# Kernel tuning notes

Hardware: AMD Instinct MI355X
Metric: run time of the kernel (lower is better)

Reference implementation:

```python
import jax, jax.numpy as jnp
import numpy as np

N = 100000
E = 3200000
IN_DIM = 512
HID = [64, 32, 16]
OUT_DIM = 40
BN_EPS = 1e-5


def setup_inputs() -> dict:
    key = jax.random.key(0)
    ks = jax.random.split(key, 10)
    x = jax.random.normal(ks[0], (N, IN_DIM), dtype=jnp.float32)
    edge_row = jnp.sort(jax.random.randint(ks[1], (E,), 0, N, dtype=jnp.int32))
    edge_col = jax.random.randint(ks[2], (E,), 0, N, dtype=jnp.int32)
    edge_val = jax.random.uniform(ks[3], (E,), dtype=jnp.float32)

    def xavier(k, fan_in, fan_out):
        limit = np.sqrt(6.0 / (fan_in + fan_out)).astype(np.float32)
        return jax.random.uniform(k, (fan_in, fan_out), dtype=jnp.float32, minval=-limit, maxval=limit)

    W1 = xavier(ks[4], IN_DIM, HID[0])
    W2 = xavier(ks[5], HID[0], HID[1])
    W3 = xavier(ks[6], HID[1], HID[2])
    W4 = xavier(ks[7], HID[2], OUT_DIM)
    return {
        "x": x, "edge_row": edge_row, "edge_col": edge_col, "edge_val": edge_val,
        "W1": W1, "W2": W2, "W3": W3, "W4": W4,
        "g1": jnp.ones((HID[0],), jnp.float32), "b1": jnp.zeros((HID[0],), jnp.float32),
        "g2": jnp.ones((HID[1],), jnp.float32), "b2": jnp.zeros((HID[1],), jnp.float32),
        "g3": jnp.ones((HID[2],), jnp.float32), "b3": jnp.zeros((HID[2],), jnp.float32),
    }


def _gcn_layer(h, W, edge_row, edge_col, edge_val, n_nodes):
    # support = h @ W  (dense GEMM), then SpMM: out[i] = sum_{e: row[e]=i} val[e] * support[col[e]]
    support = h @ W
    msgs = edge_val[:, None] * support[edge_col]  # gather + scale
    return jax.ops.segment_sum(msgs, edge_row, num_segments=n_nodes)


def _bn_elu(h, gamma, beta):
    # BatchNorm1d in training mode: batch statistics over the node dim, biased variance
    mean = jnp.mean(h, axis=0)
    var = jnp.var(h, axis=0)
    h = (h - mean) * jax.lax.rsqrt(var + BN_EPS) * gamma + beta
    return jax.nn.elu(h)


def reference(x, edge_row, edge_col, edge_val, W1, W2, W3, W4, g1, b1, g2, b2, g3, b3):
    n = x.shape[0]
    h = _gcn_layer(x, W1, edge_row, edge_col, edge_val, n)
    h = _bn_elu(h, g1, b1)  # dropout is identity in eval mode
    h = _gcn_layer(h, W2, edge_row, edge_col, edge_val, n)
    h = _bn_elu(h, g2, b2)
    h = _gcn_layer(h, W3, edge_row, edge_col, edge_val, n)
    h = _bn_elu(h, g3, b3)
    h = _gcn_layer(h, W4, edge_row, edge_col, edge_val, n)
    return jax.nn.log_softmax(h, axis=1)
```

## Files before the change

### kernel.cpp

```cpp
#include <hip/hip_runtime.h>
#include <hip/hip_bf16.h>
#include <math.h>

typedef __attribute__((ext_vector_type(8))) short short8;
typedef __attribute__((ext_vector_type(4))) float floatx4;

__global__ void rowptr_k(const int* __restrict__ erow, int* __restrict__ rp, int n, int e) {
    int i = blockIdx.x * blockDim.x + threadIdx.x;
    if (i > n) return;
    int lo = 0, hi = e;
    while (lo < hi) {
        int mid = (lo + hi) >> 1;
        if (erow[mid] < i) lo = mid + 1; else hi = mid;
    }
    rp[i] = lo;
}

__global__ void zero_k(float* __restrict__ p) {
    int i = threadIdx.x;
    if (i < 224) p[i] = 0.f;
}

__device__ __forceinline__ float elu_f(float t) {
    return t > 0.f ? t : expm1f(t);
}

__device__ __forceinline__ unsigned short f2bf(float f) {
    unsigned int u = __float_as_uint(f);
    u = (u + 0x7FFFu + ((u >> 16) & 1u)) >> 16;
    return (unsigned short)u;
}

__device__ __forceinline__ unsigned int f2bf2(float lo, float hi) {
    unsigned int a = __float_as_uint(lo);
    unsigned int b = __float_as_uint(hi);
    a = (a + 0x7FFFu + ((a >> 16) & 1u)) >> 16;
    b = (b + 0x7FFFu + ((b >> 16) & 1u)) & 0xFFFF0000u;
    return a | b;
}

__device__ __forceinline__ float bflo(unsigned int d) { return __uint_as_float(d << 16); }
__device__ __forceinline__ float bfhi(unsigned int d) { return __uint_as_float(d & 0xFFFF0000u); }

__global__ __launch_bounds__(256) void w1bf_k(const float* __restrict__ W,
                                              unsigned short* __restrict__ Wb) {
    int idx = blockIdx.x * 256 + threadIdx.x;
    int n = idx >> 9, k = idx & 511;
    Wb[idx] = f2bf(W[(long)k * 64 + n]);
}

__global__ __launch_bounds__(256) void wsmall_k(const float* __restrict__ W2,
                                                const float* __restrict__ W3,
                                                const float* __restrict__ W4,
                                                unsigned short* __restrict__ Wb2,
                                                unsigned short* __restrict__ Wb3,
                                                unsigned short* __restrict__ Wb4) {
    int idx = blockIdx.x * 256 + threadIdx.x;
    if (idx < 2048) {
        int n = idx >> 6, k = idx & 63;
        Wb2[idx] = f2bf(W2[(long)k * 32 + n]);
    }
    if (idx < 512) {
        int n = idx >> 5, k = idx & 31;
        Wb3[idx] = f2bf(W3[(long)k * 16 + n]);
    }
    if (idx < 1536) {
        int n = idx >> 5, k = idx & 31;
        Wb4[idx] = (n < 40 && k < 16) ? f2bf(W4[(long)k * 40 + n]) : (unsigned short)0;
    }
}

__global__ __launch_bounds__(256) void gemm1_mfma_k(const float* __restrict__ X,
                                                    const unsigned short* __restrict__ Wb,
                                                    unsigned short* __restrict__ out, int nrows) {
    const int lane = threadIdx.x & 63;
    const int wid  = threadIdx.x >> 6;
    const int lrow = lane & 15;
    const int quad = lane >> 4;
    const int m0   = (blockIdx.x * 4 + wid) * 16;
    if (m0 >= nrows) return;

    int arow = m0 + lrow;
    if (arow >= nrows) arow = nrows - 1;
    const float* __restrict__ xrow = X + (long)arow * 512 + quad * 8;
    const unsigned short* __restrict__ brow = Wb + lrow * 512 + quad * 8;

    floatx4 acc[4];
#pragma unroll
    for (int ni = 0; ni < 4; ++ni) acc[ni] = (floatx4){0.f, 0.f, 0.f, 0.f};

    float4 ca0 = *(const float4*)(xrow + 0);
    float4 ca1 = *(const float4*)(xrow + 4);
    short8 cb[4];
#pragma unroll
    for (int ni = 0; ni < 4; ++ni) cb[ni] = *(const short8*)(brow + ni * 8192);

#pragma unroll
    for (int kc = 0; kc < 16; ++kc) {
        float4 na0, na1;
        short8 nb[4];
        if (kc < 15) {
            const float* xp = xrow + (kc + 1) * 32;
            na0 = *(const float4*)(xp + 0);
            na1 = *(const float4*)(xp + 4);
#pragma unroll
            for (int ni = 0; ni < 4; ++ni)
                nb[ni] = *(const short8*)(brow + ni * 8192 + (kc + 1) * 32);
        }
        union { short8 s; unsigned int u[4]; } af;
        af.u[0] = f2bf2(ca0.x, ca0.y);
        af.u[1] = f2bf2(ca0.z, ca0.w);
        af.u[2] = f2bf2(ca1.x, ca1.y);
        af.u[3] = f2bf2(ca1.z, ca1.w);
#pragma unroll
        for (int ni = 0; ni < 4; ++ni)
            acc[ni] = __builtin_amdgcn_mfma_f32_16x16x32_bf16(af.s, cb[ni], acc[ni], 0, 0, 0);
        if (kc < 15) {
            ca0 = na0; ca1 = na1;
#pragma unroll
            for (int ni = 0; ni < 4; ++ni) cb[ni] = nb[ni];
        }
    }

#pragma unroll
    for (int r = 0; r < 4; ++r) {
        int gr = m0 + quad * 4 + r;
        if (gr < nrows) {
#pragma unroll
            for (int ni = 0; ni < 4; ++ni)
                out[(long)gr * 64 + ni * 16 + lrow] = f2bf(acc[ni][r]);
        }
    }
}

template<int K, int KP, int NF, int NSTR>
__global__ __launch_bounds__(256) void gemmS_k(const unsigned short* __restrict__ H,
                                               const unsigned short* __restrict__ Wb,
                                               const float* __restrict__ stats,
                                               const float* __restrict__ gamma,
                                               const float* __restrict__ beta,
                                               unsigned short* __restrict__ out,
                                               int nrows) {
    __shared__ __align__(16) float scs[K];
    __shared__ __align__(16) float shs[K];
    const int tid = threadIdx.x;
    if (tid < K) {
        float s1 = stats[tid], s2 = stats[K + tid];
        float mean = s1 / (float)nrows;
        float var  = s2 / (float)nrows - mean * mean;
        float rstd = rsqrtf(var + 1e-5f);
        float scl  = gamma[tid] * rstd;
        scs[tid] = scl;
        shs[tid] = beta[tid] - mean * scl;
    }
    __syncthreads();

    const int lane = tid & 63;
    const int wid  = tid >> 6;
    const int lrow = lane & 15;
    const int quad = lane >> 4;
    const int m0   = (blockIdx.x * 4 + wid) * 16;
    if (m0 >= nrows) return;

    int arow = m0 + lrow;
    if (arow >= nrows) arow = nrows - 1;
    const unsigned short* __restrict__ hrow = H + (long)arow * K;

    floatx4 acc[NF];
#pragma unroll
    for (int ni = 0; ni < NF; ++ni) acc[ni] = (floatx4){0.f, 0.f, 0.f, 0.f};

#pragma unroll
    for (int kc = 0; kc < KP; kc += 32) {
        const int k8 = kc + quad * 8;
        union { short8 s; unsigned int u[4]; } af;
        if (k8 < K) {
            uint4 d = *(const uint4*)(hrow + k8);
            float4 sc0 = *(const float4*)&scs[k8];
            float4 sc1 = *(const float4*)&scs[k8 + 4];
            float4 sh0 = *(const float4*)&shs[k8];
            float4 sh1 = *(const float4*)&shs[k8 + 4];
            float f0 = elu_f(bflo(d.x) * sc0.x + sh0.x);
            float f1 = elu_f(bfhi(d.x) * sc0.y + sh0.y);
            float f2 = elu_f(bflo(d.y) * sc0.z + sh0.z);
            float f3 = elu_f(bfhi(d.y) * sc0.w + sh0.w);
            float f4 = elu_f(bflo(d.z) * sc1.x + sh1.x);
            float f5 = elu_f(bfhi(d.z) * sc1.y + sh1.y);
            float f6 = elu_f(bflo(d.w) * sc1.z + sh1.z);
            float f7 = elu_f(bfhi(d.w) * sc1.w + sh1.w);
            af.u[0] = f2bf2(f0, f1);
            af.u[1] = f2bf2(f2, f3);
            af.u[2] = f2bf2(f4, f5);
            af.u[3] = f2bf2(f6, f7);
        } else {
            af.u[0] = af.u[1] = af.u[2] = af.u[3] = 0u;
        }
#pragma unroll
        for (int ni = 0; ni < NF; ++ni) {
            short8 bf = *(const short8*)&Wb[(ni * 16 + lrow) * KP + k8];
            acc[ni] = __builtin_amdgcn_mfma_f32_16x16x32_bf16(af.s, bf, acc[ni], 0, 0, 0);
        }
    }

#pragma unroll
    for (int r = 0; r < 4; ++r) {
        int gr = m0 + quad * 4 + r;
        if (gr < nrows) {
#pragma unroll
            for (int ni = 0; ni < NF; ++ni)
                out[(long)gr * NSTR + ni * 16 + lrow] = f2bf(acc[ni][r]);
        }
    }
}

template<int F>
__global__ __launch_bounds__(256) void spmmb_k(const int* __restrict__ rp,
                                               const int* __restrict__ ecol,
                                               const float* __restrict__ ev,
                                               const unsigned short* __restrict__ sup,
                                               unsigned short* __restrict__ out, int n) {
    constexpr int GL = F / 4;
    constexpr int G  = 64 / GL;
    const int lane = threadIdx.x & 63;
    const int node = (blockIdx.x * blockDim.x + threadIdx.x) >> 6;
    if (node >= n) return;
    int s = __builtin_amdgcn_readfirstlane(rp[node]);
    int e = __builtin_amdgcn_readfirstlane(rp[node + 1]);
    const int g = lane / GL, p = lane % GL;
    float a0 = 0.f, a1 = 0.f, a2 = 0.f, a3 = 0.f;
    for (int i = s; i < e; i += 4 * G) {
#pragma unroll
        for (int b = 0; b < 4; ++b) {
            int idx = i + b * G + g;
            int cidx = idx < e ? idx : e - 1;
            int col = ecol[cidx];
            float v = ev[cidx];
            if (idx >= e) v = 0.f;
            uint2 d = *(const uint2*)((const char*)sup + (unsigned long long)col * (F * 2) + p * 8);
            a0 += v * bflo(d.x);
            a1 += v * bfhi(d.x);
            a2 += v * bflo(d.y);
            a3 += v * bfhi(d.y);
        }
    }
#pragma unroll
    for (int o = GL; o < 64; o <<= 1) {
        a0 += __shfl_xor(a0, o, 64);
        a1 += __shfl_xor(a1, o, 64);
        a2 += __shfl_xor(a2, o, 64);
        a3 += __shfl_xor(a3, o, 64);
    }
    if (lane < GL) {
        ushort4 o4;
        o4.x = f2bf(a0); o4.y = f2bf(a1); o4.z = f2bf(a2); o4.w = f2bf(a3);
        *(ushort4*)&out[(long)node * F + p * 4] = o4;
    }
}

__global__ __launch_bounds__(256) void spmm4b_k(const int* __restrict__ rp,
                                                const int* __restrict__ ecol,
                                                const float* __restrict__ ev,
                                                const unsigned short* __restrict__ sup,
                                                float* __restrict__ out, int n) {
    const int lane = threadIdx.x & 63;
    const int node = (blockIdx.x * blockDim.x + threadIdx.x) >> 6;
    if (node >= n) return;
    int s = __builtin_amdgcn_readfirstlane(rp[node]);
    int e = __builtin_amdgcn_readfirstlane(rp[node + 1]);
    const int g = lane >> 4, p = lane & 15;
    float a0 = 0.f, a1 = 0.f, a2 = 0.f, a3 = 0.f;
    for (int i = s; i < e; i += 16) {
#pragma unroll
        for (int b = 0; b < 4; ++b) {
            int idx = i + b * 4 + g;
            int cidx = idx < e ? idx : e - 1;
            int col = ecol[cidx];
            float v = ev[cidx];
            if (idx >= e || p >= 12) v = 0.f;
            uint2 d = *(const uint2*)((const char*)sup + (unsigned long long)col * 96 + p * 8);
            a0 += v * bflo(d.x);
            a1 += v * bfhi(d.x);
            a2 += v * bflo(d.y);
            a3 += v * bfhi(d.y);
        }
    }
#pragma unroll
    for (int o = 16; o < 64; o <<= 1) {
        a0 += __shfl_xor(a0, o, 64);
        a1 += __shfl_xor(a1, o, 64);
        a2 += __shfl_xor(a2, o, 64);
        a3 += __shfl_xor(a3, o, 64);
    }
    const bool valid = p < 10;
    float lm = valid ? fmaxf(fmaxf(a0, a1), fmaxf(a2, a3)) : -INFINITY;
#pragma unroll
    for (int o = 1; o < 16; o <<= 1) lm = fmaxf(lm, __shfl_xor(lm, o, 64));
    float ls = valid ? (expf(a0 - lm) + expf(a1 - lm) + expf(a2 - lm) + expf(a3 - lm)) : 0.f;
#pragma unroll
    for (int o = 1; o < 16; o <<= 1) ls += __shfl_xor(ls, o, 64);
    float lse = lm + logf(ls);
    if (lane < 10) {
        float4 o4 = make_float4(a0 - lse, a1 - lse, a2 - lse, a3 - lse);
        *(float4*)&out[(long)node * 40 + p * 4] = o4;
    }
}

template<int F>
__global__ __launch_bounds__(256) void statsb_k(const unsigned short* __restrict__ h,
                                                float* __restrict__ stats, int n) {
    __shared__ float m1[256], m2[256], m3[256], m4[256];
    const int tid = threadIdx.x;
    const unsigned int* h2 = (const unsigned int*)h;
    const long total = (long)n * F / 2;
    float s1 = 0.f, s2 = 0.f, t1 = 0.f, t2 = 0.f;
    for (long idx = (long)blockIdx.x * 256 + tid; idx < total; idx += (long)gridDim.x * 256) {
        unsigned int d = h2[idx];
        float lo = bflo(d), hi = bfhi(d);
        s1 += lo; s2 += lo * lo;
        t1 += hi; t2 += hi * hi;
    }
    m1[tid] = s1; m2[tid] = s2; m3[tid] = t1; m4[tid] = t2;
    __syncthreads();
    if (tid < F / 2) {
#pragma unroll 4
        for (int j = 1; j < 256 / (F / 2); ++j) {
            s1 += m1[tid + j * (F / 2)];
            s2 += m2[tid + j * (F / 2)];
            t1 += m3[tid + j * (F / 2)];
            t2 += m4[tid + j * (F / 2)];
        }
        atomicAdd(&stats[2 * tid], s1);
        atomicAdd(&stats[2 * tid + 1], t1);
        atomicAdd(&stats[F + 2 * tid], s2);
        atomicAdd(&stats[F + 2 * tid + 1], t2);
    }
}

extern "C" void kernel_launch(void* const* d_in, const int* in_sizes, int n_in,
                              void* d_out, int out_size, void* d_ws, size_t ws_size,
                              hipStream_t stream) {
    const float* x    = (const float*)d_in[0];
    const int*   erow = (const int*)d_in[1];
    const int*   ecol = (const int*)d_in[2];
    const float* ev   = (const float*)d_in[3];
    const float* W1   = (const float*)d_in[4];
    const float* W2   = (const float*)d_in[5];
    const float* W3   = (const float*)d_in[6];
    const float* W4   = (const float*)d_in[7];
    const float* g1   = (const float*)d_in[8];
    const float* b1   = (const float*)d_in[9];
    const float* g2   = (const float*)d_in[10];
    const float* b2   = (const float*)d_in[11];
    const float* g3   = (const float*)d_in[12];
    const float* b3   = (const float*)d_in[13];

    const int N = in_sizes[0] / 512;
    const int E = in_sizes[1];

    char* w = (char*)d_ws;
    int* rp = (int*)w;
    size_t off = (((size_t)(N + 1) * 4) + 255) & ~(size_t)255;
    float* stats = (float*)(w + off);
    unsigned short* Abf = (unsigned short*)(stats + 256);
    unsigned short* Bbf = Abf + (size_t)N * 64;
    unsigned short* Wb1 = Bbf + (size_t)N * 64;
    unsigned short* Wb2 = Wb1 + 64 * 512;
    unsigned short* Wb3 = Wb2 + 32 * 64;
    unsigned short* Wb4 = Wb3 + 16 * 32;
    float* outp = (float*)d_out;

    rowptr_k<<<(N + 1 + 255) / 256, 256, 0, stream>>>(erow, rp, N, E);
    zero_k<<<1, 256, 0, stream>>>(stats);
    w1bf_k<<<128, 256, 0, stream>>>(W1, Wb1);
    wsmall_k<<<8, 256, 0, stream>>>(W2, W3, W4, Wb2, Wb3, Wb4);

    const int mblocks = ((N + 15) / 16 + 3) / 4;
    const int sblocks = (N * 64 + 255) / 256;

    gemm1_mfma_k<<<mblocks, 256, 0, stream>>>(x, Wb1, Abf, N);
    spmmb_k<64><<<sblocks, 256, 0, stream>>>(rp, ecol, ev, Abf, Bbf, N);
    statsb_k<64><<<512, 256, 0, stream>>>(Bbf, stats, N);

    gemmS_k<64, 64, 2, 32><<<mblocks, 256, 0, stream>>>(Bbf, Wb2, stats, g1, b1, Abf, N);
    spmmb_k<32><<<sblocks, 256, 0, stream>>>(rp, ecol, ev, Abf, Bbf, N);
    statsb_k<32><<<512, 256, 0, stream>>>(Bbf, stats + 128, N);

    gemmS_k<32, 32, 1, 16><<<mblocks, 256, 0, stream>>>(Bbf, Wb3, stats + 128, g2, b2, Abf, N);
    spmmb_k<16><<<sblocks, 256, 0, stream>>>(rp, ecol, ev, Abf, Bbf, N);
    statsb_k<16><<<512, 256, 0, stream>>>(Bbf, stats + 192, N);

    gemmS_k<16, 32, 3, 48><<<mblocks, 256, 0, stream>>>(Bbf, Wb4, stats + 192, g3, b3, Abf, N);
    spmm4b_k<<<sblocks, 256, 0, stream>>>(rp, ecol, ev, Abf, outp, N);
}
```

Before: 668.8 us.

## Reorder last layer to aggregate 16-wide features before applying W4

The final layer now runs the sparse aggregation on the 16-wide BN+ELU activations, with normalization fused into the gather, and applies W4 plus log-softmax afterwards in a small dense kernel. This uses (A·h)·W = A·(h·W), so each edge gathers 32 bytes per neighbour instead of 96 and the padded 48-wide support GEMM is no longer needed. In exchange, ELU and the BN affine are recomputed for every gathered edge, and a 16-wide float intermediate is written and read back. Edge processing widens to 16 edges per iteration, with 4 lanes per edge.

Result: slower. 683.6 us (+2.2%).

```diff
diff --git a/kernel.cpp b/kernel.cpp
--- a/kernel.cpp
+++ b/kernel.cpp
@@ -51,10 +51,8 @@
 
 __global__ __launch_bounds__(256) void wsmall_k(const float* __restrict__ W2,
                                                 const float* __restrict__ W3,
-                                                const float* __restrict__ W4,
                                                 unsigned short* __restrict__ Wb2,
-                                                unsigned short* __restrict__ Wb3,
-                                                unsigned short* __restrict__ Wb4) {
+                                                unsigned short* __restrict__ Wb3) {
     int idx = blockIdx.x * 256 + threadIdx.x;
     if (idx < 2048) {
         int n = idx >> 6, k = idx & 63;
@@ -63,10 +61,6 @@
     if (idx < 512) {
         int n = idx >> 5, k = idx & 31;
         Wb3[idx] = f2bf(W3[(long)k * 16 + n]);
-    }
-    if (idx < 1536) {
-        int n = idx >> 5, k = idx & 31;
-        Wb4[idx] = (n < 40 && k < 16) ? f2bf(W4[(long)k * 40 + n]) : (unsigned short)0;
     }
 }
 
@@ -257,40 +251,87 @@
     }
 }
 
-__global__ __launch_bounds__(256) void spmm4b_k(const int* __restrict__ rp,
-                                                const int* __restrict__ ecol,
-                                                const float* __restrict__ ev,
-                                                const unsigned short* __restrict__ sup,
-                                                float* __restrict__ out, int n) {
+__global__ __launch_bounds__(256) void spmmf16_k(const int* __restrict__ rp,
+                                                 const int* __restrict__ ecol,
+                                                 const float* __restrict__ ev,
+                                                 const unsigned short* __restrict__ h,
+                                                 const float* __restrict__ stats,
+                                                 const float* __restrict__ gamma,
+                                                 const float* __restrict__ beta,
+                                                 float* __restrict__ out, int n) {
     const int lane = threadIdx.x & 63;
     const int node = (blockIdx.x * blockDim.x + threadIdx.x) >> 6;
     if (node >= n) return;
+    const int g = lane >> 2, p = lane & 3;
+    float scl[4], sh[4];
+#pragma unroll
+    for (int j = 0; j < 4; ++j) {
+        int c = p * 4 + j;
+        float s1 = stats[c], s2 = stats[16 + c];
+        float mean = s1 / (float)n;
+        float var  = s2 / (float)n - mean * mean;
+        float rstd = rsqrtf(var + 1e-5f);
+        scl[j] = gamma[c] * rstd;
+        sh[j]  = beta[c] - mean * scl[j];
+    }
     int s = __builtin_amdgcn_readfirstlane(rp[node]);
     int e = __builtin_amdgcn_readfirstlane(rp[node + 1]);
-    const int g = lane >> 4, p = lane & 15;
     float a0 = 0.f, a1 = 0.f, a2 = 0.f, a3 = 0.f;
-    for (int i = s; i < e; i += 16) {
+    for (int i = s; i < e; i += 64) {
 #pragma unroll
         for (int b = 0; b < 4; ++b) {
-            int idx = i + b * 4 + g;
+            int idx = i + b * 16 + g;
             int cidx = idx < e ? idx : e - 1;
             int col = ecol[cidx];
             float v = ev[cidx];
-            if (idx >= e || p >= 12) v = 0.f;
-            uint2 d = *(const uint2*)((const char*)sup + (unsigned long long)col * 96 + p * 8);
-            a0 += v * bflo(d.x);
-            a1 += v * bfhi(d.x);
-            a2 += v * bflo(d.y);
-            a3 += v * bfhi(d.y);
-        }
-    }
-#pragma unroll
-    for (int o = 16; o < 64; o <<= 1) {
+            if (idx >= e) v = 0.f;
+            uint2 d = *(const uint2*)((const char*)h + (unsigned long long)col * 32 + p * 8);
+            a0 += v * elu_f(bflo(d.x) * scl[0] + sh[0]);
+            a1 += v * elu_f(bfhi(d.x) * scl[1] + sh[1]);
+            a2 += v * elu_f(bflo(d.y) * scl[2] + sh[2]);
+            a3 += v * elu_f(bfhi(d.y) * scl[3] + sh[3]);
+        }
+    }
+#pragma unroll
+    for (int o = 4; o < 64; o <<= 1) {
         a0 += __shfl_xor(a0, o, 64);
         a1 += __shfl_xor(a1, o, 64);
         a2 += __shfl_xor(a2, o, 64);
         a3 += __shfl_xor(a3, o, 64);
     }
+    if (lane < 4) {
+        float4 o4 = make_float4(a0, a1, a2, a3);
+        *(float4*)&out[(long)node * 16 + p * 4] = o4;
+    }
+}
+
+__global__ __launch_bounds__(256) void gemm4ls_k(const float* __restrict__ T,
+                                                 const float* __restrict__ W4,
+                                                 float* __restrict__ out, int n) {
+    __shared__ __align__(16) float w[16 * 64];
+    const int tid = threadIdx.x;
+    for (int i = tid; i < 1024; i += 256) {
+        int k = i >> 6, c = i & 63;
+        w[i] = (c < 40) ? W4[k * 40 + c] : 0.f;
+    }
+    __syncthreads();
+    const int grp = tid >> 4;
+    const int p   = tid & 15;
+    const int row = blockIdx.x * 16 + grp;
+    if (row >= n) return;
+    const float4* tp = (const float4*)(T + (long)row * 16);
+    float4 t0 = tp[0], t1 = tp[1], t2 = tp[2], t3 = tp[3];
+    float h[16] = {t0.x, t0.y, t0.z, t0.w, t1.x, t1.y, t1.z, t1.w,
+                   t2.x, t2.y, t2.z, t2.w, t3.x, t3.y, t3.z, t3.w};
+    float a0 = 0.f, a1 = 0.f, a2 = 0.f, a3 = 0.f;
+#pragma unroll
+    for (int k = 0; k < 16; ++k) {
+        float4 wv = *(const float4*)&w[k * 64 + p * 4];
+        a0 += h[k] * wv.x;
+        a1 += h[k] * wv.y;
+        a2 += h[k] * wv.z;
+        a3 += h[k] * wv.w;
+    }
     const bool valid = p < 10;
     float lm = valid ? fmaxf(fmaxf(a0, a1), fmaxf(a2, a3)) : -INFINITY;
 #pragma unroll
@@ -299,9 +340,9 @@
 #pragma unroll
     for (int o = 1; o < 16; o <<= 1) ls += __shfl_xor(ls, o, 64);
     float lse = lm + logf(ls);
-    if (lane < 10) {
+    if (valid) {
         float4 o4 = make_float4(a0 - lse, a1 - lse, a2 - lse, a3 - lse);
-        *(float4*)&out[(long)node * 40 + p * 4] = o4;
+        *(float4*)&out[(long)row * 40 + p * 4] = o4;
     }
 }
 
@@ -366,13 +407,13 @@
     unsigned short* Wb1 = Bbf + (size_t)N * 64;
     unsigned short* Wb2 = Wb1 + 64 * 512;
     unsigned short* Wb3 = Wb2 + 32 * 64;
-    unsigned short* Wb4 = Wb3 + 16 * 32;
+    float* Tf = (float*)Abf;
     float* outp = (float*)d_out;
 
     rowptr_k<<<(N + 1 + 255) / 256, 256, 0, stream>>>(erow, rp, N, E);
     zero_k<<<1, 256, 0, stream>>>(stats);
     w1bf_k<<<128, 256, 0, stream>>>(W1, Wb1);
-    wsmall_k<<<8, 256, 0, stream>>>(W2, W3, W4, Wb2, Wb3, Wb4);
+    wsmall_k<<<8, 256, 0, stream>>>(W2, W3, Wb2, Wb3);
 
     const int mblocks = ((N + 15) / 16 + 3) / 4;
     const int sblocks = (N * 64 + 255) / 256;
@@ -389,6 +430,6 @@
     spmmb_k<16><<<sblocks, 256, 0, stream>>>(rp, ecol, ev, Abf, Bbf, N);
     statsb_k<16><<<512, 256, 0, stream>>>(Bbf, stats + 192, N);
 
-    gemmS_k<16, 32, 3, 48><<<mblocks, 256, 0, stream>>>(Bbf, Wb4, stats + 192, g3, b3, Abf, N);
-    spmm4b_k<<<sblocks, 256, 0, stream>>>(rp, ecol, ev, Abf, outp, N);
-}
+    spmmf16_k<<<sblocks, 256, 0, stream>>>(rp, ecol, ev, Bbf, stats + 192, g3, b3, Tf, N);
+    gemm4ls_k<<<(N + 15) / 16, 256, 0, stream>>>(Tf, W4, outp, N);
+}
```
